# Kernel tuning notes

Hardware: AMD Instinct MI355X
Metric: run time of the kernel (lower is better)

The kernel has to match this reference:

```python
import jax, jax.numpy as jnp
import numpy as np

PUSH_MARGIN = 1.0
NUM_LABELS = 65  # label ids 0..64; 0 = background (skipped)
EPS = 1e-12


def _safe_norm(d, axis):
    # L2 norm with grad-safe sqrt at 0 (matches ||.||_2 value everywhere relevant)
    sq = jnp.sum(d * d, axis=axis)
    return jnp.sqrt(jnp.maximum(sq, EPS))


def setup_inputs() -> dict:
    key = jax.random.key(0)
    k1, k2, k3 = jax.random.split(key, 3)
    B, N, C, H, W = 16, 16384, 128, 512, 512
    abs_embedding = jax.random.normal(k1, (B, N, C), dtype=jnp.float32)
    coordinates = jax.random.randint(k2, (B, N, 2), 0, H, dtype=jnp.int32)
    y = jax.random.randint(k3, (B, H, W), 0, NUM_LABELS, dtype=jnp.int32)
    return {"abs_embedding": abs_embedding, "coordinates": coordinates, "y": y}


def reference(abs_embedding, coordinates, y):
    def per_image(emb, coords, yb):
        # emb: [N,C], coords: [N,2], yb: [H,W]
        labels = yb[coords[:, 0], coords[:, 1]]                       # [N]
        ones = jnp.ones(labels.shape, emb.dtype)
        counts = jax.ops.segment_sum(ones, labels, num_segments=NUM_LABELS)   # [L]
        sums = jax.ops.segment_sum(emb, labels, num_segments=NUM_LABELS)      # [L,C]
        centroids = sums / jnp.maximum(counts, 1.0)[:, None]                   # [L,C]
        # pull: per-instance mean distance of samples to their centroid, summed over fg instances
        d = _safe_norm(emb - centroids[labels], axis=-1)              # [N]
        dist_sum = jax.ops.segment_sum(d, labels, num_segments=NUM_LABELS)
        fg_counts = counts[1:]
        present = fg_counts > 0
        pull = jnp.sum(jnp.where(present, dist_sum[1:] / jnp.maximum(fg_counts, 1.0), 0.0))
        # push: mean over strict-upper-tri pairs of relu(margin - ||c_i - c_j||)
        c = centroids[1:]                                             # [K,C]
        dm = _safe_norm(c[:, None, :] - c[None, :, :], axis=-1)        # [K,K]
        push_vals = jax.nn.relu(PUSH_MARGIN - dm)
        K = c.shape[0]
        tri = jnp.triu(jnp.ones((K, K), bool), k=1)
        pair_mask = tri & present[:, None] & present[None, :]
        npairs = jnp.maximum(jnp.sum(pair_mask.astype(emb.dtype)), 1.0)
        push = jnp.sum(jnp.where(pair_mask, push_vals, 0.0)) / npairs
        return pull + push

    per_b = jax.vmap(per_image)(abs_embedding, coordinates, y)        # [B]
    return jnp.sum(per_b)
```

## Files before the change

### kernel.cpp

```cpp
#include <hip/hip_runtime.h>

#define B_ 16
#define N_ 16384
#define C_ 128
#define H_ 512
#define W_ 512
#define L_ 65
#define FG 64

#define OFF_SUMS 0
#define OFF_CNT  (B_*L_*C_)
#define OFF_DIST (OFF_CNT + B_*L_)
#define OFF_LAB  (OFF_DIST + B_*L_)

#define APB 512
#define DPB 512

__global__ __launch_bounds__(256) void k_zero(float* __restrict__ ws, float* __restrict__ out) {
    int i = blockIdx.x * 256 + threadIdx.x;
    if (i < OFF_LAB) ws[i] = 0.f;
    if (i == 0) out[0] = 0.f;
}

__global__ __launch_bounds__(256) void k_labels(const int2* __restrict__ coords,
                                                const int* __restrict__ y,
                                                float* __restrict__ ws) {
    __shared__ float s_cnt[L_];
    int t = blockIdx.x * 256 + threadIdx.x;
    int b = t >> 14;
    if (threadIdx.x < L_) s_cnt[threadIdx.x] = 0.f;
    __syncthreads();
    int2 rc = coords[t];
    int lab = y[(b << 18) + (rc.x << 9) + rc.y];
    ((int*)(ws + OFF_LAB))[t] = lab;
    atomicAdd(&s_cnt[lab], 1.f);
    __syncthreads();
    if (threadIdx.x < L_) {
        float c = s_cnt[threadIdx.x];
        if (c != 0.f) unsafeAtomicAdd(ws + OFF_CNT + b * L_ + threadIdx.x, c);
    }
}

__global__ __launch_bounds__(256) void k_accum(const float* __restrict__ emb,
                                               float* __restrict__ ws) {
    __shared__ float s_sum[2 * L_ * C_];
    __shared__ int s_lab[APB];
    const int b = blockIdx.x >> 5;
    const int base = (blockIdx.x & 31) * APB;
    const int wave = threadIdx.x >> 6;
    const int lane = threadIdx.x & 63;
    const int half = lane >> 5, j = lane & 31;
    const int ch = 32 * wave + j;

    for (int i = threadIdx.x; i < 2 * L_ * C_; i += 256) s_sum[i] = 0.f;
    const int* labg = (const int*)(ws + OFF_LAB) + b * N_ + base;
    for (int i = threadIdx.x; i < APB; i += 256) s_lab[i] = labg[i];
    __syncthreads();

    const float* embp = emb + (size_t)b * N_ * C_ + (size_t)base * C_ + ch;
    float* copy = s_sum + half * (L_ * C_);

    for (int s0 = 0; s0 < APB / 2; s0 += 8) {
        float e[8]; int lb[8];
        #pragma unroll
        for (int u = 0; u < 8; ++u) {
            int p = 2 * (s0 + u) + half;
            e[u]  = embp[(size_t)p * C_];
            lb[u] = s_lab[p];
        }
        #pragma unroll
        for (int u = 0; u < 8; ++u) {
            copy[lb[u] * C_ + ch] += e[u];
        }
    }
    __syncthreads();
    float* gs = ws + OFF_SUMS + b * L_ * C_;
    for (int i = threadIdx.x; i < L_ * C_; i += 256)
        unsafeAtomicAdd(&gs[i], s_sum[i] + s_sum[L_ * C_ + i]);
}

__global__ __launch_bounds__(256) void k_final_cent(float* __restrict__ ws) {
    int i = blockIdx.x * 256 + threadIdx.x;
    if (i >= B_ * L_ * C_) return;
    float cnt = ws[OFF_CNT + (i / C_)];
    ws[OFF_SUMS + i] = ws[OFF_SUMS + i] / fmaxf(cnt, 1.f);
}

__global__ __launch_bounds__(256) void k_dist(const float* __restrict__ emb,
                                              float* __restrict__ ws) {
    __shared__ __align__(16) float4 s_cent4[L_ * 33];
    __shared__ float s_dist[L_];
    const int b = blockIdx.x >> 5;
    const int base = (blockIdx.x & 31) * DPB;

    const float* gcent = ws + OFF_SUMS + b * L_ * C_;
    for (int i = threadIdx.x; i < L_ * 32; i += 256) {
        int l = i >> 5, q = i & 31;
        s_cent4[l * 33 + q] = ((const float4*)gcent)[l * 32 + q];
    }
    if (threadIdx.x < L_) s_dist[threadIdx.x] = 0.f;
    __syncthreads();

    const int* labg = (const int*)(ws + OFF_LAB) + b * N_ + base;
    const float4* embp = (const float4*)(emb + (size_t)b * N_ * C_ + (size_t)base * C_);

    for (int it = 0; it < DPB; it += 256) {
        int p = it + threadIdx.x;
        int lb = labg[p];
        const float4* ep = embp + (size_t)p * 32;
        const float4* cp = s_cent4 + lb * 33;
        float acc = 0.f;
        #pragma unroll 8
        for (int q = 0; q < 32; ++q) {
            float4 e = ep[q], c = cp[q];
            float dx = e.x - c.x, dy = e.y - c.y;
            float dz = e.z - c.z, dw = e.w - c.w;
            acc += dx * dx + dy * dy + dz * dz + dw * dw;
        }
        atomicAdd(&s_dist[lb], sqrtf(fmaxf(acc, 1e-12f)));
    }
    __syncthreads();
    if (threadIdx.x < L_) {
        float d = s_dist[threadIdx.x];
        if (d != 0.f) unsafeAtomicAdd(ws + OFF_DIST + b * L_ + threadIdx.x, d);
    }
}

#define CSTRIDE 132

__global__ __launch_bounds__(256) void k_final(float* __restrict__ ws, float* __restrict__ out) {
    __shared__ __align__(16) float s_cc[FG * CSTRIDE];
    __shared__ float s_present[FG];
    __shared__ float s_red[3];
    const int b = blockIdx.x;
    const int t = threadIdx.x;

    const float* gcent = ws + OFF_SUMS + b * L_ * C_;
    for (int i = t; i < FG * C_; i += 256) {
        int l = i >> 7, ch = i & 127;
        s_cc[l * CSTRIDE + ch] = gcent[(l + 1) * C_ + ch];
    }
    if (t < 3) s_red[t] = 0.f;
    if (t < FG) {
        float cnt = ws[OFF_CNT + b * L_ + 1 + t];
        s_present[t] = (cnt > 0.f) ? 1.f : 0.f;
        float pl = (cnt > 0.f) ? ws[OFF_DIST + b * L_ + 1 + t] / cnt : 0.f;
        #pragma unroll
        for (int off = 32; off; off >>= 1) pl += __shfl_xor(pl, off);
        if (t == 0) s_red[0] = pl;
    }
    __syncthreads();

    const int wave = t >> 6, lane = t & 63;
    const int ti = lane >> 3, tj = lane & 7;
    float psum = 0.f, pnp = 0.f;
    for (int tt = wave; tt < 36; tt += 4) {
        int a = 0, c = tt;
        while (c >= 8 - a) { c -= 8 - a; ++a; }
        c += a;
        int i = a * 8 + ti, jx = c * 8 + tj;
        float acc = 0.f;
        #pragma unroll
        for (int ch = 0; ch < C_; ch += 4) {
            float4 xi = *(const float4*)&s_cc[i * CSTRIDE + ch];
            float4 xj = *(const float4*)&s_cc[jx * CSTRIDE + ch];
            float dx = xi.x - xj.x, dy = xi.y - xj.y;
            float dz = xi.z - xj.z, dw = xi.w - xj.w;
            acc += dx * dx + dy * dy + dz * dz + dw * dw;
        }
        float dm = sqrtf(fmaxf(acc, 1e-12f));
        float pv = fmaxf(1.f - dm, 0.f);
        bool valid = (i < jx) && (s_present[i] > 0.f) && (s_present[jx] > 0.f);
        if (valid) { psum += pv; pnp += 1.f; }
    }
    #pragma unroll
    for (int off = 32; off; off >>= 1) {
        psum += __shfl_xor(psum, off);
        pnp  += __shfl_xor(pnp,  off);
    }
    if (lane == 0) { unsafeAtomicAdd(&s_red[1], psum); unsafeAtomicAdd(&s_red[2], pnp); }
    __syncthreads();
    if (t == 0) {
        float loss = s_red[0] + s_red[1] / fmaxf(s_red[2], 1.f);
        unsafeAtomicAdd(out, loss);
    }
}

extern "C" void kernel_launch(void* const* d_in, const int* in_sizes, int n_in,
                              void* d_out, int out_size, void* d_ws, size_t ws_size,
                              hipStream_t stream) {
    const float* emb   = (const float*)d_in[0];
    const int2* coords = (const int2*)d_in[1];
    const int*  y      = (const int*)d_in[2];
    float* out = (float*)d_out;
    float* ws  = (float*)d_ws;

    k_zero<<<(OFF_LAB + 255) / 256, 256, 0, stream>>>(ws, out);
    k_labels<<<(B_ * N_) / 256, 256, 0, stream>>>(coords, y, ws);
    k_accum<<<B_ * (N_ / APB), 256, 0, stream>>>(emb, ws);
    k_final_cent<<<(B_ * L_ * C_ + 255) / 256, 256, 0, stream>>>(ws);
    k_dist<<<B_ * (N_ / DPB), 256, 0, stream>>>(emb, ws);
    k_final<<<B_, 256, 0, stream>>>(ws, out);
}
```

Measured before the change: 259.6 us.

## Fuse zeroing into label kernel, per-block counts, and retune accum/dist sizes

Merges the workspace-zeroing kernel into the label-gather kernel, dropping one launch. Per-label counts are now written as per-block integer partials instead of global float atomics, and a new per-image kernel reduces them while normalizing the centroids. The accumulate loop unroll goes from 8 to 16, and the distance kernel now uses 256 points per block, doubling the grid. The catch is that zeroing relies on the prep grid covering the whole sums region, and the extra partial-count buffer adds a serial reduction inside a kernel that launches only 16 blocks.

```diff
diff --git a/kernel.cpp b/kernel.cpp
--- a/kernel.cpp
+++ b/kernel.cpp
@@ -12,33 +12,31 @@
 #define OFF_CNT  (B_*L_*C_)
 #define OFF_DIST (OFF_CNT + B_*L_)
 #define OFF_LAB  (OFF_DIST + B_*L_)
+#define OFF_BCNT (OFF_LAB + B_*N_)
 
 #define APB 512
-#define DPB 512
-
-__global__ __launch_bounds__(256) void k_zero(float* __restrict__ ws, float* __restrict__ out) {
-    int i = blockIdx.x * 256 + threadIdx.x;
-    if (i < OFF_LAB) ws[i] = 0.f;
-    if (i == 0) out[0] = 0.f;
-}
-
-__global__ __launch_bounds__(256) void k_labels(const int2* __restrict__ coords,
-                                                const int* __restrict__ y,
-                                                float* __restrict__ ws) {
-    __shared__ float s_cnt[L_];
-    int t = blockIdx.x * 256 + threadIdx.x;
-    int b = t >> 14;
-    if (threadIdx.x < L_) s_cnt[threadIdx.x] = 0.f;
-    __syncthreads();
-    int2 rc = coords[t];
+#define DPB 256
+#define PREP_BLOCKS (B_*N_/256)
+
+__global__ __launch_bounds__(256) void k_prep(const int2* __restrict__ coords,
+                                              const int* __restrict__ y,
+                                              float* __restrict__ ws,
+                                              float* __restrict__ out) {
+    __shared__ int s_cnt[L_];
+    const int gid = blockIdx.x * 256 + threadIdx.x;
+    if (threadIdx.x < L_) s_cnt[threadIdx.x] = 0;
+    if (gid < OFF_CNT) ws[gid] = 0.f;
+    if (gid < B_ * L_) ws[OFF_DIST + gid] = 0.f;
+    if (gid == 0) out[0] = 0.f;
+    __syncthreads();
+    const int b = gid >> 14;
+    int2 rc = coords[gid];
     int lab = y[(b << 18) + (rc.x << 9) + rc.y];
-    ((int*)(ws + OFF_LAB))[t] = lab;
-    atomicAdd(&s_cnt[lab], 1.f);
-    __syncthreads();
-    if (threadIdx.x < L_) {
-        float c = s_cnt[threadIdx.x];
-        if (c != 0.f) unsafeAtomicAdd(ws + OFF_CNT + b * L_ + threadIdx.x, c);
-    }
+    ((int*)(ws + OFF_LAB))[gid] = lab;
+    atomicAdd(&s_cnt[lab], 1);
+    __syncthreads();
+    if (threadIdx.x < L_)
+        ((int*)(ws + OFF_BCNT))[blockIdx.x * L_ + threadIdx.x] = s_cnt[threadIdx.x];
 }
 
 __global__ __launch_bounds__(256) void k_accum(const float* __restrict__ emb,
@@ -60,18 +58,17 @@
     const float* embp = emb + (size_t)b * N_ * C_ + (size_t)base * C_ + ch;
     float* copy = s_sum + half * (L_ * C_);
 
-    for (int s0 = 0; s0 < APB / 2; s0 += 8) {
-        float e[8]; int lb[8];
-        #pragma unroll
-        for (int u = 0; u < 8; ++u) {
+    for (int s0 = 0; s0 < APB / 2; s0 += 16) {
+        float e[16]; int lb[16];
+        #pragma unroll
+        for (int u = 0; u < 16; ++u) {
             int p = 2 * (s0 + u) + half;
             e[u]  = embp[(size_t)p * C_];
             lb[u] = s_lab[p];
         }
         #pragma unroll
-        for (int u = 0; u < 8; ++u) {
+        for (int u = 0; u < 16; ++u)
             copy[lb[u] * C_ + ch] += e[u];
-        }
     }
     __syncthreads();
     float* gs = ws + OFF_SUMS + b * L_ * C_;
@@ -79,19 +76,30 @@
         unsafeAtomicAdd(&gs[i], s_sum[i] + s_sum[L_ * C_ + i]);
 }
 
-__global__ __launch_bounds__(256) void k_final_cent(float* __restrict__ ws) {
-    int i = blockIdx.x * 256 + threadIdx.x;
-    if (i >= B_ * L_ * C_) return;
-    float cnt = ws[OFF_CNT + (i / C_)];
-    ws[OFF_SUMS + i] = ws[OFF_SUMS + i] / fmaxf(cnt, 1.f);
+__global__ __launch_bounds__(256) void k_cent(float* __restrict__ ws) {
+    __shared__ float s_inv[L_];
+    const int b = blockIdx.x;
+    const int t = threadIdx.x;
+    if (t < L_) {
+        const int* bc = (const int*)(ws + OFF_BCNT);
+        int c = 0;
+        #pragma unroll 8
+        for (int k = 0; k < PREP_BLOCKS / B_; ++k)
+            c += bc[(b * (PREP_BLOCKS / B_) + k) * L_ + t];
+        ((int*)(ws + OFF_CNT))[b * L_ + t] = c;
+        s_inv[t] = 1.f / fmaxf((float)c, 1.f);
+    }
+    __syncthreads();
+    float* gs = ws + OFF_SUMS + b * L_ * C_;
+    for (int i = t; i < L_ * C_; i += 256) gs[i] *= s_inv[i >> 7];
 }
 
 __global__ __launch_bounds__(256) void k_dist(const float* __restrict__ emb,
                                               float* __restrict__ ws) {
     __shared__ __align__(16) float4 s_cent4[L_ * 33];
     __shared__ float s_dist[L_];
-    const int b = blockIdx.x >> 5;
-    const int base = (blockIdx.x & 31) * DPB;
+    const int b = blockIdx.x >> 6;
+    const int base = (blockIdx.x & 63) * DPB;
 
     const float* gcent = ws + OFF_SUMS + b * L_ * C_;
     for (int i = threadIdx.x; i < L_ * 32; i += 256) {
@@ -101,24 +109,19 @@
     if (threadIdx.x < L_) s_dist[threadIdx.x] = 0.f;
     __syncthreads();
 
-    const int* labg = (const int*)(ws + OFF_LAB) + b * N_ + base;
-    const float4* embp = (const float4*)(emb + (size_t)b * N_ * C_ + (size_t)base * C_);
-
-    for (int it = 0; it < DPB; it += 256) {
-        int p = it + threadIdx.x;
-        int lb = labg[p];
-        const float4* ep = embp + (size_t)p * 32;
-        const float4* cp = s_cent4 + lb * 33;
-        float acc = 0.f;
-        #pragma unroll 8
-        for (int q = 0; q < 32; ++q) {
-            float4 e = ep[q], c = cp[q];
-            float dx = e.x - c.x, dy = e.y - c.y;
-            float dz = e.z - c.z, dw = e.w - c.w;
-            acc += dx * dx + dy * dy + dz * dz + dw * dw;
-        }
-        atomicAdd(&s_dist[lb], sqrtf(fmaxf(acc, 1e-12f)));
-    }
+    const int p = base + threadIdx.x;
+    const int lb = ((const int*)(ws + OFF_LAB))[b * N_ + p];
+    const float4* ep = (const float4*)(emb + (size_t)b * N_ * C_) + (size_t)p * 32;
+    const float4* cp = s_cent4 + lb * 33;
+    float acc = 0.f;
+    #pragma unroll 8
+    for (int q = 0; q < 32; ++q) {
+        float4 e = ep[q], c = cp[q];
+        float dx = e.x - c.x, dy = e.y - c.y;
+        float dz = e.z - c.z, dw = e.w - c.w;
+        acc += dx * dx + dy * dy + dz * dz + dw * dw;
+    }
+    unsafeAtomicAdd(&s_dist[lb], sqrtf(fmaxf(acc, 1e-12f)));
     __syncthreads();
     if (threadIdx.x < L_) {
         float d = s_dist[threadIdx.x];
@@ -142,9 +145,9 @@
     }
     if (t < 3) s_red[t] = 0.f;
     if (t < FG) {
-        float cnt = ws[OFF_CNT + b * L_ + 1 + t];
-        s_present[t] = (cnt > 0.f) ? 1.f : 0.f;
-        float pl = (cnt > 0.f) ? ws[OFF_DIST + b * L_ + 1 + t] / cnt : 0.f;
+        int cnt = ((const int*)(ws + OFF_CNT))[b * L_ + 1 + t];
+        s_present[t] = (cnt > 0) ? 1.f : 0.f;
+        float pl = (cnt > 0) ? ws[OFF_DIST + b * L_ + 1 + t] / (float)cnt : 0.f;
         #pragma unroll
         for (int off = 32; off; off >>= 1) pl += __shfl_xor(pl, off);
         if (t == 0) s_red[0] = pl;
@@ -195,10 +198,9 @@
     float* out = (float*)d_out;
     float* ws  = (float*)d_ws;
 
-    k_zero<<<(OFF_LAB + 255) / 256, 256, 0, stream>>>(ws, out);
-    k_labels<<<(B_ * N_) / 256, 256, 0, stream>>>(coords, y, ws);
+    k_prep<<<PREP_BLOCKS, 256, 0, stream>>>(coords, y, ws, out);
     k_accum<<<B_ * (N_ / APB), 256, 0, stream>>>(emb, ws);
-    k_final_cent<<<(B_ * L_ * C_ + 255) / 256, 256, 0, stream>>>(ws);
+    k_cent<<<B_, 256, 0, stream>>>(ws);
     k_dist<<<B_ * (N_ / DPB), 256, 0, stream>>>(emb, ws);
     k_final<<<B_, 256, 0, stream>>>(ws, out);
 }
```

Result: no change. 261.5 us (+0.7%).
